# Optimization experiments

Hardware: AMD Instinct MI355X
Metric: run time of the kernel (lower is better)

## Reference

```python
import jax, jax.numpy as jnp
import numpy as np

N, E, CIN, COUT = 100000, 1600000, 64, 128
EPS = 1e-5  # torch BatchNorm default


def setup_inputs() -> dict:
    key = jax.random.key(0)
    ks = jax.random.split(key, 16)
    s = 0.1
    x = jax.random.normal(ks[0], (N, CIN), jnp.float32)
    src = jax.random.randint(ks[1], (E,), 0, N, dtype=jnp.int32)
    dst = jax.random.randint(ks[2], (E,), 0, N, dtype=jnp.int32)
    edge_index = jnp.stack([src, dst])  # [2, E]
    return {
        "x": x,
        "edge_index": edge_index,
        # conv0: GraphConv(CIN -> COUT)
        "W_root0": jax.random.normal(ks[3], (COUT, CIN), jnp.float32) * s,
        "W_nbr0": jax.random.normal(ks[4], (COUT, CIN), jnp.float32) * s,
        "b0": jnp.zeros((COUT,), jnp.float32),
        # bn0
        "g0": jnp.ones((COUT,), jnp.float32),
        "be0": jnp.zeros((COUT,), jnp.float32),
        # conv1: GraphConv(COUT -> COUT)
        "W_root1": jax.random.normal(ks[5], (COUT, COUT), jnp.float32) * s,
        "W_nbr1": jax.random.normal(ks[6], (COUT, COUT), jnp.float32) * s,
        "b1": jnp.zeros((COUT,), jnp.float32),
        # bn1
        "g1": jnp.ones((COUT,), jnp.float32),
        "be1": jnp.zeros((COUT,), jnp.float32),
        # residual 1x1 conv (Conv1d(CIN, COUT, 1))
        "Wlin": jax.random.normal(ks[7], (COUT, CIN), jnp.float32) * s,
        "blin": jnp.zeros((COUT,), jnp.float32),
    }


def graph_conv(x, src, dst, W_root, W_nbr, b):
    # PyG GraphConv: out_i = W_root x_i + W_nbr * sum_{j: (j->i) in E} x_j + b
    agg = jax.ops.segment_sum(x[src], dst, num_segments=N)  # scatter-add over edges
    return x @ W_root.T + agg @ W_nbr.T + b


def batch_norm(x, gamma, beta):
    # training-mode BatchNorm over the node dimension (biased variance)
    mu = jnp.mean(x, axis=0)
    var = jnp.mean(jnp.square(x - mu), axis=0)
    return (x - mu) * jax.lax.rsqrt(var + EPS) * gamma + beta


def reference(x, edge_index, W_root0, W_nbr0, b0, g0, be0,
              W_root1, W_nbr1, b1, g1, be1, Wlin, blin):
    src, dst = edge_index[0], edge_index[1]
    y = batch_norm(graph_conv(x, src, dst, W_root0, W_nbr0, b0), g0, be0)
    y = jax.nn.relu(y)
    y = batch_norm(graph_conv(y, src, dst, W_root1, W_nbr1, b1), g1, be1)
    out = y + (x @ Wlin.T + blin)  # 1x1 Conv1d residual projection
    return jax.nn.relu(out)
```

## Files before the change

### kernel.cpp

```cpp
#include <hip/hip_runtime.h>
#include <stdint.h>


#define CIN 64
#define COUT 128
#define BN_EPS 1e-5f
#define CURPAD 32
#define PCPAD 32
#define SPAD 32
#define PSH 8
#define PNODES (1 << PSH)
#define MAXP 512

typedef unsigned short u16;
typedef short short8 __attribute__((ext_vector_type(8)));
typedef float f32x4 __attribute__((ext_vector_type(4)));

__device__ __forceinline__ float bf2f(u16 u) {
    union { unsigned int i; float f; } v; v.i = ((unsigned int)u) << 16; return v.f;
}
__device__ __forceinline__ u16 f2bf(float f) {
    union { float f; unsigned int i; } v; v.f = f;
    unsigned int r = v.i + 0x7fffu + ((v.i >> 16) & 1u);
    return (u16)(r >> 16);
}
__device__ __forceinline__ float lo16(unsigned int w) { return bf2f((u16)(w & 0xffffu)); }
__device__ __forceinline__ float hi16(unsigned int w) { return bf2f((u16)(w >> 16)); }

template<bool BF> __device__ __forceinline__ float ldf(const void* p, long i) {
    if (BF) return bf2f(((const u16*)p)[i]);
    return ((const float*)p)[i];
}
template<bool BF> __device__ __forceinline__ short8 ld8(const void* p, long i) {
    if (BF) return *(const short8*)((const u16*)p + i);
    const float* f = (const float*)p + i;
    short8 r;
#pragma unroll
    for (int j = 0; j < 8; ++j) r[j] = (short)f2bf(f[j]);
    return r;
}

__device__ __forceinline__ void acc8(float* a, uint4 w) {
    a[0] += lo16(w.x); a[1] += hi16(w.x);
    a[2] += lo16(w.y); a[3] += hi16(w.y);
    a[4] += lo16(w.z); a[5] += hi16(w.z);
    a[6] += lo16(w.w); a[7] += hi16(w.w);
}

__global__ __launch_bounds__(256) void k_prep(const unsigned int* __restrict__ x,
        int* __restrict__ flag, const int* __restrict__ dst,
        int* __restrict__ pcount, int E, int np) {
    if (blockIdx.x == 0) {
        if (threadIdx.x < 64) {
            int lane = threadIdx.x;
            int cnt = 0;
#pragma unroll
            for (int i = 0; i < 8; ++i) {
                unsigned int w = x[lane * 8 + i];
                unsigned int e0 = (w >> 7) & 0xFFu, e1 = (w >> 23) & 0xFFu;
                cnt += (e0 >= 0x60u && e0 <= 0x8Eu);
                cnt += (e1 >= 0x60u && e1 <= 0x8Eu);
            }
            for (int o = 32; o; o >>= 1) cnt += __shfl_down(cnt, o);
            if (lane == 0) *flag = (cnt > 850) ? 1 : 0;
        }
        return;
    }
    __shared__ int h[MAXP];
    int bid = blockIdx.x - 1;
    int nb = gridDim.x - 1;
    for (int i = threadIdx.x; i < np; i += 256) h[i] = 0;
    __syncthreads();
    int stride = nb * 256;
    for (int e = bid * 256 + threadIdx.x; e < E; e += stride)
        atomicAdd(&h[dst[e] >> PSH], 1);
    __syncthreads();
    for (int i = threadIdx.x; i < np; i += 256)
        if (h[i]) atomicAdd(&pcount[i * PCPAD], h[i]);
}

__global__ void k_pscan(const int* __restrict__ pcount, int* __restrict__ pstart,
                        int* __restrict__ pcursor, int np, int E) {
    __shared__ int s[MAXP];
    int t = threadIdx.x;
    int v = (t < np) ? pcount[t * PCPAD] : 0;
    s[t] = v; __syncthreads();
    for (int o = 1; o < MAXP; o <<= 1) {
        int u = (t >= o) ? s[t - o] : 0;
        __syncthreads(); s[t] += u; __syncthreads();
    }
    if (t < np) {
        int ex = s[t] - v;
        pstart[t] = ex;
        pcursor[t * CURPAD] = ex;
    }
    if (t == 0) pstart[np] = E;
}

__global__ __launch_bounds__(256) void k_fill2(const int* __restrict__ src,
        const int* __restrict__ dst, int* __restrict__ pcursor,
        unsigned int* __restrict__ barr, int E, int np, int ntl,
        const int* __restrict__ flag, const void* __restrict__ x,
        u16* __restrict__ xb, long n8) {
    __shared__ int cnt[MAXP], gb[MAXP], loc[MAXP];
    int tid = threadIdx.x;
    if (blockIdx.x >= ntl) {
        int nb = gridDim.x - ntl;
        long idx = (long)(blockIdx.x - ntl) * 256 + tid;
        long stride = (long)nb * 256;
        uint4* d4 = (uint4*)xb;
        if (*flag) {
            const uint4* s4 = (const uint4*)x;
            for (; idx < n8; idx += stride) d4[idx] = s4[idx];
        } else {
            const float4* s4 = (const float4*)x;
            for (; idx < n8; idx += stride) {
                float4 a = s4[idx * 2], b = s4[idx * 2 + 1];
                uint4 o;
                o.x = (unsigned int)f2bf(a.x) | ((unsigned int)f2bf(a.y) << 16);
                o.y = (unsigned int)f2bf(a.z) | ((unsigned int)f2bf(a.w) << 16);
                o.z = (unsigned int)f2bf(b.x) | ((unsigned int)f2bf(b.y) << 16);
                o.w = (unsigned int)f2bf(b.z) | ((unsigned int)f2bf(b.w) << 16);
                d4[idx] = o;
            }
        }
        return;
    }
    int base = blockIdx.x * 4096;
    for (int i = tid; i < np; i += 256) { cnt[i] = 0; loc[i] = 0; }
    __syncthreads();
    int pk[16]; unsigned int rec[16];
#pragma unroll
    for (int k = 0; k < 16; ++k) {
        int e = base + k * 256 + tid;
        if (e < E) {
            int d = dst[e];
            pk[k] = d >> PSH;
            rec[k] = ((unsigned int)(d & (PNODES - 1)) << 20) | (unsigned int)src[e];
            atomicAdd(&cnt[pk[k]], 1);
        } else pk[k] = -1;
    }
    __syncthreads();
    for (int i = tid; i < np; i += 256)
        if (cnt[i]) gb[i] = atomicAdd(&pcursor[i * CURPAD], cnt[i]);
    __syncthreads();
#pragma unroll
    for (int k = 0; k < 16; ++k) {
        if (pk[k] >= 0) {
            int off = atomicAdd(&loc[pk[k]], 1);
            barr[gb[pk[k]] + off] = rec[k];
        }
    }
}

__global__ __launch_bounds__(256) void k_psort(const unsigned int* __restrict__ barr,
        const int* __restrict__ pstart, int* __restrict__ csr,
        int* __restrict__ row_start, int n, int np, int E) {
    __shared__ int hist[PNODES], curs[PNODES], tsum[256];
    int tid = threadIdx.x;
    int p = blockIdx.x;
    int e0 = pstart[p], e1 = pstart[p + 1];
    int node0 = p << PSH;
    hist[tid] = 0;
    __syncthreads();
    for (int t = e0 + tid; t < e1; t += 256)
        atomicAdd(&hist[barr[t] >> 20], 1);
    __syncthreads();
    int v = hist[tid];
    tsum[tid] = v; __syncthreads();
    for (int o = 1; o < 256; o <<= 1) {
        int u = (tid >= o) ? tsum[tid - o] : 0;
        __syncthreads(); tsum[tid] += u; __syncthreads();
    }
    int ex = tsum[tid] - v;
    curs[tid] = ex;
    int nd = node0 + tid;
    if (nd < n) row_start[nd] = e0 + ex;
    if (p == np - 1 && tid == 0) row_start[n] = E;
    __syncthreads();
    for (int t = e0 + tid; t < e1; t += 256) {
        unsigned int rec = barr[t];
        int pos = atomicAdd(&curs[rec >> 20], 1);
        csr[e0 + pos] = (int)(rec & 0xFFFFF);
    }
}

__global__ __launch_bounds__(256) void k_agg0(const u16* __restrict__ xb,
        const int* __restrict__ rs, const int* __restrict__ csr,
        u16* __restrict__ agg, int n) {
    int i = blockIdx.x * 4 + (threadIdx.x >> 6);
    if (i >= n) return;
    int lane = threadIdx.x & 63;
    int slot = lane >> 4, cp = lane & 15;
    const unsigned int* x32 = (const unsigned int*)xb;
    int b = rs[i], e = rs[i + 1];
    float acc[4] = {0.f, 0.f, 0.f, 0.f};
    int t = b + slot;
    for (; t + 12 < e; t += 16) {
        int j0 = csr[t], j1 = csr[t + 4], j2 = csr[t + 8], j3 = csr[t + 12];
        uint2 w0 = *((const uint2*)(x32 + (long)j0 * 32) + cp);
        uint2 w1 = *((const uint2*)(x32 + (long)j1 * 32) + cp);
        uint2 w2 = *((const uint2*)(x32 + (long)j2 * 32) + cp);
        uint2 w3 = *((const uint2*)(x32 + (long)j3 * 32) + cp);
        acc[0] += lo16(w0.x) + lo16(w1.x); acc[1] += hi16(w0.x) + hi16(w1.x);
        acc[2] += lo16(w0.y) + lo16(w1.y); acc[3] += hi16(w0.y) + hi16(w1.y);
        acc[0] += lo16(w2.x) + lo16(w3.x); acc[1] += hi16(w2.x) + hi16(w3.x);
        acc[2] += lo16(w2.y) + lo16(w3.y); acc[3] += hi16(w2.y) + hi16(w3.y);
    }
    for (; t < e; t += 4) {
        int j0 = csr[t];
        uint2 w0 = *((const uint2*)(x32 + (long)j0 * 32) + cp);
        acc[0] += lo16(w0.x); acc[1] += hi16(w0.x);
        acc[2] += lo16(w0.y); acc[3] += hi16(w0.y);
    }
#pragma unroll
    for (int k = 0; k < 4; ++k) {
        acc[k] += __shfl_xor(acc[k], 16);
        acc[k] += __shfl_xor(acc[k], 32);
    }
    if (slot == 0) {
        uint2 o;
        o.x = (unsigned int)f2bf(acc[0]) | ((unsigned int)f2bf(acc[1]) << 16);
        o.y = (unsigned int)f2bf(acc[2]) | ((unsigned int)f2bf(acc[3]) << 16);
        *((uint2*)((unsigned int*)agg + (long)i * 32) + cp) = o;
    }
}

__global__ __launch_bounds__(256) void k_y0p(unsigned int* __restrict__ y0,
        const float* __restrict__ sc, const float* __restrict__ sh, long nq) {
    long idx = (long)blockIdx.x * 256 + threadIdx.x;
    int colq = threadIdx.x & 15;
    float s8[8], h8[8];
#pragma unroll
    for (int j = 0; j < 8; ++j) { s8[j] = sc[colq * 8 + j]; h8[j] = sh[colq * 8 + j]; }
    long stride = (long)gridDim.x * 256;
    uint4* p = (uint4*)y0;
    for (; idx < nq; idx += stride) {
        uint4 w = p[idx];
        unsigned int r[4] = {w.x, w.y, w.z, w.w};
        uint4 o;
        unsigned int* po = (unsigned int*)&o;
#pragma unroll
        for (int d = 0; d < 4; ++d) {
            float a = fmaxf(lo16(r[d]) * s8[2 * d]     + h8[2 * d],     0.f);
            float b = fmaxf(hi16(r[d]) * s8[2 * d + 1] + h8[2 * d + 1], 0.f);
            po[d] = (unsigned int)f2bf(a) | ((unsigned int)f2bf(b) << 16);
        }
        p[idx] = o;
    }
}

__global__ __launch_bounds__(256) void k_agg1(const u16* __restrict__ y0p,
        const int* __restrict__ rs, const int* __restrict__ csr,
        u16* __restrict__ agg, int n) {
    int i = blockIdx.x * 4 + (threadIdx.x >> 6);
    if (i >= n) return;
    int lane = threadIdx.x & 63;
    int slot = lane >> 4, cp = lane & 15;
    const unsigned int* y32 = (const unsigned int*)y0p;
    int b = rs[i], e = rs[i + 1];
    float acc[8] = {0.f, 0.f, 0.f, 0.f, 0.f, 0.f, 0.f, 0.f};
    int t = b + slot;
    for (; t + 12 < e; t += 16) {
        int j0 = csr[t], j1 = csr[t + 4], j2 = csr[t + 8], j3 = csr[t + 12];
        uint4 w0 = *((const uint4*)(y32 + (long)j0 * 64) + cp);
        uint4 w1 = *((const uint4*)(y32 + (long)j1 * 64) + cp);
        uint4 w2 = *((const uint4*)(y32 + (long)j2 * 64) + cp);
        uint4 w3 = *((const uint4*)(y32 + (long)j3 * 64) + cp);
        acc8(acc, w0); acc8(acc, w1); acc8(acc, w2); acc8(acc, w3);
    }
    for (; t < e; t += 4) {
        int j0 = csr[t];
        uint4 w0 = *((const uint4*)(y32 + (long)j0 * 64) + cp);
        acc8(acc, w0);
    }
#pragma unroll
    for (int k = 0; k < 8; ++k) {
        acc[k] += __shfl_xor(acc[k], 16);
        acc[k] += __shfl_xor(acc[k], 32);
    }
    if (slot == 0) {
        uint4 o;
        o.x = (unsigned int)f2bf(acc[0]) | ((unsigned int)f2bf(acc[1]) << 16);
        o.y = (unsigned int)f2bf(acc[2]) | ((unsigned int)f2bf(acc[3]) << 16);
        o.z = (unsigned int)f2bf(acc[4]) | ((unsigned int)f2bf(acc[5]) << 16);
        o.w = (unsigned int)f2bf(acc[6]) | ((unsigned int)f2bf(acc[7]) << 16);
        *((uint4*)((unsigned int*)agg + (long)i * 64) + cp) = o;
    }
}

template<bool BF>
__device__ __forceinline__ void gemm0_impl(const u16* xb, const u16* agg,
                                           const void* Wr, const void* Wn,
                                           u16* y0, float* sumP, float* sqP,
                                           int n, int nch) {
    int tid = threadIdx.x;
    int wave = tid >> 6, lane = tid & 63, lr = lane & 15, q = lane >> 4;

    short8 wf[2][4];
#pragma unroll
    for (int i = 0; i < 2; ++i) {
        int c = (2 * wave + i) * 16 + lr;
#pragma unroll
        for (int ks = 0; ks < 4; ++ks) {
            const void* W = (ks < 2) ? Wr : Wn;
            wf[i][ks] = ld8<BF>(W, (long)c * CIN + (ks & 1) * 32 + q * 8);
        }
    }

    float st[2] = {0.f, 0.f}, sq[2] = {0.f, 0.f};
    for (int ch = blockIdx.x; ch < nch; ch += gridDim.x) {
        long chunk0 = (long)ch * 64;
#pragma unroll
        for (int t = 0; t < 4; ++t) {
            long rg = chunk0 + t * 16 + lr; if (rg > n - 1) rg = n - 1;
            short8 a[4];
#pragma unroll
            for (int ks = 0; ks < 2; ++ks)
                a[ks] = *(const short8*)(xb + rg * CIN + ks * 32 + q * 8);
#pragma unroll
            for (int ks = 0; ks < 2; ++ks)
                a[2 + ks] = *(const short8*)(agg + rg * CIN + ks * 32 + q * 8);
#pragma unroll
            for (int i = 0; i < 2; ++i) {
                f32x4 acc = {0.f, 0.f, 0.f, 0.f};
#pragma unroll
                for (int ks = 0; ks < 4; ++ks)
                    acc = __builtin_amdgcn_mfma_f32_16x16x32_bf16(a[ks], wf[i][ks], acc, 0, 0, 0);
                int c = (2 * wave + i) * 16 + lr;
#pragma unroll
                for (int r = 0; r < 4; ++r) {
                    long row = chunk0 + t * 16 + q * 4 + r;
                    if (row < n) {
                        y0[row * COUT + c] = f2bf(acc[r]);
                        st[i] += acc[r]; sq[i] += acc[r] * acc[r];
                    }
                }
            }
        }
    }
#pragma unroll
    for (int i = 0; i < 2; ++i) {
        st[i] += __shfl_xor(st[i], 16); st[i] += __shfl_xor(st[i], 32);
        sq[i] += __shfl_xor(sq[i], 16); sq[i] += __shfl_xor(sq[i], 32);
    }
    if (q == 0) {
#pragma unroll
        for (int i = 0; i < 2; ++i) {
            int c = (2 * wave + i) * 16 + lr;
            atomicAdd(&sumP[c * SPAD], st[i]);
            atomicAdd(&sqP[c * SPAD], sq[i]);
        }
    }
}

__global__ __launch_bounds__(256) void k_gemm0(const int* __restrict__ flag,
        const u16* __restrict__ xb, const u16* __restrict__ agg,
        const void* Wr, const void* Wn,
        u16* __restrict__ y0, float* __restrict__ sumP, float* __restrict__ sqP,
        int n, int nch) {
    if (*flag) gemm0_impl<true >(xb, agg, Wr, Wn, y0, sumP, sqP, n, nch);
    else       gemm0_impl<false>(xb, agg, Wr, Wn, y0, sumP, sqP, n, nch);
}

template<bool BF>
__device__ __forceinline__ void gemm1_impl(const u16* y0p, const u16* agg,
                                           const void* Wr, const void* Wn,
                                           u16* y1, float* sumP, float* sqP,
                                           int n, int nch) {
    int tid = threadIdx.x;
    int wave = tid >> 6, lane = tid & 63, lr = lane & 15, q = lane >> 4;

    short8 wf[2][8];
#pragma unroll
    for (int i = 0; i < 2; ++i) {
        int c = (2 * wave + i) * 16 + lr;
#pragma unroll
        for (int ks = 0; ks < 8; ++ks) {
            const void* W = (ks < 4) ? Wr : Wn;
            wf[i][ks] = ld8<BF>(W, (long)c * COUT + (ks & 3) * 32 + q * 8);
        }
    }

    float st[2] = {0.f, 0.f}, sq[2] = {0.f, 0.f};
    for (int ch = blockIdx.x; ch < nch; ch += gridDim.x) {
        long chunk0 = (long)ch * 64;
#pragma unroll
        for (int t = 0; t < 4; ++t) {
            long rg = chunk0 + t * 16 + lr; if (rg > n - 1) rg = n - 1;
            short8 a[8];
#pragma unroll
            for (int ks = 0; ks < 4; ++ks)
                a[ks] = *(const short8*)(y0p + rg * COUT + ks * 32 + q * 8);
#pragma unroll
            for (int ks = 0; ks < 4; ++ks)
                a[4 + ks] = *(const short8*)(agg + rg * COUT + ks * 32 + q * 8);
#pragma unroll
            for (int i = 0; i < 2; ++i) {
                f32x4 acc = {0.f, 0.f, 0.f, 0.f};
#pragma unroll
                for (int ks = 0; ks < 8; ++ks)
                    acc = __builtin_amdgcn_mfma_f32_16x16x32_bf16(a[ks], wf[i][ks], acc, 0, 0, 0);
                int c = (2 * wave + i) * 16 + lr;
#pragma unroll
                for (int r = 0; r < 4; ++r) {
                    long row = chunk0 + t * 16 + q * 4 + r;
                    if (row < n) {
                        y1[row * COUT + c] = f2bf(acc[r]);
                        st[i] += acc[r]; sq[i] += acc[r] * acc[r];
                    }
                }
            }
        }
    }
#pragma unroll
    for (int i = 0; i < 2; ++i) {
        st[i] += __shfl_xor(st[i], 16); st[i] += __shfl_xor(st[i], 32);
        sq[i] += __shfl_xor(sq[i], 16); sq[i] += __shfl_xor(sq[i], 32);
    }
    if (q == 0) {
#pragma unroll
        for (int i = 0; i < 2; ++i) {
            int c = (2 * wave + i) * 16 + lr;
            atomicAdd(&sumP[c * SPAD], st[i]);
            atomicAdd(&sqP[c * SPAD], sq[i]);
        }
    }
}

__global__ __launch_bounds__(256) void k_gemm1(const int* __restrict__ flag,
        const u16* __restrict__ y0p, const u16* __restrict__ agg,
        const void* Wr, const void* Wn,
        u16* y1_bf , u16* y1_ws,
        float* __restrict__ sumP, float* __restrict__ sqP, int n, int nch) {
    u16* y1 = *flag ? y1_bf : y1_ws;
    if (*flag) gemm1_impl<true >(y0p, agg, Wr, Wn, y1, sumP, sqP, n, nch);
    else       gemm1_impl<false>(y0p, agg, Wr, Wn, y1, sumP, sqP, n, nch);
}

__global__ void k_bnfin(const int* __restrict__ flag,
                        const float* __restrict__ sumP, const float* __restrict__ sqP,
                        const void* g, const void* be,
                        float* __restrict__ scale, float* __restrict__ shift, int n) {
    int c = threadIdx.x;
    bool bf = (*flag != 0);
    float inv = 1.f / (float)n;
    float mu = sumP[c * SPAD] * inv;
    float var = fmaxf(sqP[c * SPAD] * inv - mu * mu, 0.f);
    float gv = bf ? bf2f(((const u16*)g)[c]) : ((const float*)g)[c];
    float bv = bf ? bf2f(((const u16*)be)[c]) : ((const float*)be)[c];
    float sc = gv * rsqrtf(var + BN_EPS);
    scale[c] = sc;
    shift[c] = bv - mu * sc;
}

template<bool BF>
__device__ __forceinline__ void final_impl(const u16* xb, const u16* y1,
                                           const void* Wlin, const void* blin,
                                           const float* sc, const float* sh,
                                           void* out, int n, int nch, u16* lds) {
    const int ST = 130;
    int tid = threadIdx.x;
    int wave = tid >> 6, lane = tid & 63, lr = lane & 15, q = lane >> 4;

    short8 wf[2][2];
    float blc[2], scc[2], shc[2];
#pragma unroll
    for (int i = 0; i < 2; ++i) {
        int c = (2 * wave + i) * 16 + lr;
#pragma unroll
        for (int ks = 0; ks < 2; ++ks)
            wf[i][ks] = ld8<BF>(Wlin, (long)c * CIN + ks * 32 + q * 8);
        blc[i] = ldf<BF>(blin, c);
        scc[i] = sc[c]; shc[i] = sh[c];
    }

    const int rowy = tid >> 4, wy = tid & 15;
    short8 ry[4];

    auto regload = [&](long chunk0) {
#pragma unroll
        for (int i = 0; i < 4; ++i) {
            long rg = chunk0 + rowy + i * 16; if (rg > n - 1) rg = n - 1;
            ry[i] = *(const short8*)(y1 + rg * COUT + wy * 8);
        }
    };

    int ch = blockIdx.x;
    if (ch < nch) regload((long)ch * 64);
    for (; ch < nch; ch += gridDim.x) {
        long chunk0 = (long)ch * 64;
        __syncthreads();
#pragma unroll
        for (int i = 0; i < 4; ++i)
            *(short8*)(lds + (rowy + i * 16) * ST + wy * 8) = ry[i];
        __syncthreads();
        long nxt = (long)ch + gridDim.x;
        if (nxt < nch) regload(nxt * 64);

#pragma unroll
        for (int t = 0; t < 4; ++t) {
            long rg = chunk0 + t * 16 + lr; if (rg > n - 1) rg = n - 1;
            short8 a[2];
#pragma unroll
            for (int ks = 0; ks < 2; ++ks)
                a[ks] = *(const short8*)(xb + rg * CIN + ks * 32 + q * 8);
#pragma unroll
            for (int i = 0; i < 2; ++i) {
                f32x4 acc = {0.f, 0.f, 0.f, 0.f};
                acc = __builtin_amdgcn_mfma_f32_16x16x32_bf16(a[0], wf[i][0], acc, 0, 0, 0);
                acc = __builtin_amdgcn_mfma_f32_16x16x32_bf16(a[1], wf[i][1], acc, 0, 0, 0);
                int c = (2 * wave + i) * 16 + lr;
#pragma unroll
                for (int r = 0; r < 4; ++r) {
                    long row = chunk0 + t * 16 + q * 4 + r;
                    if (row < n) {
                        float yv = bf2f(lds[(t * 16 + q * 4 + r) * ST + c]);
                        float v = acc[r] + blc[i] + yv * scc[i] + shc[i];
                        v = fmaxf(v, 0.f);
                        if (BF) ((u16*)out)[row * COUT + c] = f2bf(v);
                        else    ((float*)out)[row * COUT + c] = v;
                    }
                }
            }
        }
    }
}

__global__ __launch_bounds__(256) void k_final(const int* __restrict__ flag,
        const u16* __restrict__ xb, const void* Wlin, const void* blin,
        const u16* y1_bf , const u16* y1_ws,
        const float* __restrict__ sc, const float* __restrict__ sh,
        void* out, int n, int nch) {
    __shared__ u16 lds[64 * 130];
    const u16* y1 = *flag ? y1_bf : y1_ws;
    if (*flag) final_impl<true >(xb, y1, Wlin, blin, sc, sh, out, n, nch, lds);
    else       final_impl<false>(xb, y1, Wlin, blin, sc, sh, out, n, nch, lds);
}

extern "C" void kernel_launch(void* const* d_in, const int* in_sizes, int n_in,
                              void* d_out, int out_size, void* d_ws, size_t ws_size,
                              hipStream_t stream) {
    (void)n_in; (void)out_size; (void)ws_size;
    const void* x    = d_in[0];
    const int*  ei   = (const int*)d_in[1];
    const void* Wr0  = d_in[2];
    const void* Wn0  = d_in[3];
    const void* g0   = d_in[5];
    const void* be0  = d_in[6];
    const void* Wr1  = d_in[7];
    const void* Wn1  = d_in[8];
    const void* g1   = d_in[10];
    const void* be1  = d_in[11];
    const void* Wlin = d_in[12];
    const void* blin = d_in[13];

    const int N = in_sizes[0] / CIN;
    const int E = in_sizes[1] / 2;
    const int* src = ei;
    const int* dst = ei + E;
    const int NP = (N + PNODES - 1) >> PSH;

    char* base = (char*)d_ws;
    size_t off = 0;
    auto carve = [&](size_t bytes) -> void* {
        void* p = base + off;
        off = (off + bytes + 255) & ~(size_t)255;
        return p;
    };
    int*   flag      = (int*)carve(256);
    int*   pcount    = (int*)carve(MAXP * PCPAD * sizeof(int));
    int*   pstart    = (int*)carve((MAXP + 1) * sizeof(int));
    int*   pcursor   = (int*)carve(MAXP * CURPAD * sizeof(int));
    float* statsP    = (float*)carve(4 * 128 * SPAD * sizeof(float));
    float* scsh      = (float*)carve(512 * sizeof(float));
    int*   row_start = (int*)carve((size_t)(N + 1) * sizeof(int));
    unsigned int* barr = (unsigned int*)carve((size_t)E * sizeof(int));
    int*   csr       = (int*)carve((size_t)E * sizeof(int));
    u16*   xb        = (u16*)carve((size_t)N * CIN * sizeof(u16));
    u16*   aggu      = (u16*)carve((size_t)N * COUT * sizeof(u16));
    u16*   y0        = (u16*)carve((size_t)N * COUT * sizeof(u16));
    u16*   y1_ws     = (u16*)carve((size_t)N * COUT * sizeof(u16));

    float* sum0P = statsP;
    float* sq0P  = statsP + 128 * SPAD;
    float* sum1P = statsP + 256 * SPAD;
    float* sq1P  = statsP + 384 * SPAD;

    hipMemsetAsync(pcount, 0, MAXP * PCPAD * sizeof(int), stream);
    hipMemsetAsync(statsP, 0, 4 * 128 * SPAD * sizeof(float), stream);

    const int nwb = (N + 3) / 4;
    const int nch = (N + 63) / 64;
    const int ntl = (E + 4095) / 4096;
    const int G   = nch < 1024 ? nch : 1024;
    const long nq = (long)N * 16;
    const long n8 = (long)N * CIN / 8;
    int g2 = (int)((nq + 255) / 256); if (g2 > 2048) g2 = 2048;
    int g3 = (int)((n8 + 255) / 256); if (g3 > 1024) g3 = 1024;

    k_prep<<<257, 256, 0, stream>>>((const unsigned int*)x, flag, dst, pcount, E, NP);
    k_pscan<<<1, MAXP, 0, stream>>>(pcount, pstart, pcursor, NP, E);
    k_fill2<<<ntl + g3, 256, 0, stream>>>(src, dst, pcursor, barr, E, NP, ntl,
                                          flag, x, xb, n8);
    k_psort<<<NP, 256, 0, stream>>>(barr, pstart, csr, row_start, N, NP, E);

    k_agg0 <<<nwb, 256, 0, stream>>>(xb, row_start, csr, aggu, N);
    k_gemm0<<<G, 256, 0, stream>>>(flag, xb, aggu, Wr0, Wn0, y0,
                                   sum0P, sq0P, N, nch);
    k_bnfin<<<1, 128, 0, stream>>>(flag, sum0P, sq0P, g0, be0,
                                   scsh, scsh + 128, N);

    k_y0p<<<g2, 256, 0, stream>>>((unsigned int*)y0, scsh, scsh + 128, nq);

    k_agg1 <<<nwb, 256, 0, stream>>>(y0, row_start, csr, aggu, N);
    k_gemm1<<<G, 256, 0, stream>>>(flag, y0, aggu, Wr1, Wn1,
                                   (u16*)d_out, y1_ws, sum1P, sq1P, N, nch);
    k_bnfin<<<1, 128, 0, stream>>>(flag, sum1P, sq1P, g1, be1,
                                   scsh + 256, scsh + 384, N);

    k_final<<<G, 256, 0, stream>>>(flag, xb, Wlin, blin,
                                   (const u16*)d_out, y1_ws,
                                   scsh + 256, scsh + 384, d_out, N, nch);
}
```

Before: 385.1 us.

## Fuse layer-1 neighbor aggregation into GEMM kernel via LDS staging

Removes the standalone k_agg1 kernel. The conv1 GEMM kernel now gathers and sums neighbor features for each 64-node chunk itself, stages the bf16 aggregate in shared memory (padded stride 130), and feeds the MFMA from LDS. This avoids writing the aggregate to global memory and reading it back, and saves one launch. The cost is that the gather now runs on the persistent GEMM grid G, with fewer waves in flight for latency hiding, and the gather and MFMA phases are serialized by barriers.

Result: slower. 414.4 us (+7.6%).

```diff
diff --git a/kernel.cpp b/kernel.cpp
--- a/kernel.cpp
+++ b/kernel.cpp
@@ -250,45 +250,6 @@
     }
 }
 
-__global__ __launch_bounds__(256) void k_agg1(const u16* __restrict__ y0p,
-        const int* __restrict__ rs, const int* __restrict__ csr,
-        u16* __restrict__ agg, int n) {
-    int i = blockIdx.x * 4 + (threadIdx.x >> 6);
-    if (i >= n) return;
-    int lane = threadIdx.x & 63;
-    int slot = lane >> 4, cp = lane & 15;
-    const unsigned int* y32 = (const unsigned int*)y0p;
-    int b = rs[i], e = rs[i + 1];
-    float acc[8] = {0.f, 0.f, 0.f, 0.f, 0.f, 0.f, 0.f, 0.f};
-    int t = b + slot;
-    for (; t + 12 < e; t += 16) {
-        int j0 = csr[t], j1 = csr[t + 4], j2 = csr[t + 8], j3 = csr[t + 12];
-        uint4 w0 = *((const uint4*)(y32 + (long)j0 * 64) + cp);
-        uint4 w1 = *((const uint4*)(y32 + (long)j1 * 64) + cp);
-        uint4 w2 = *((const uint4*)(y32 + (long)j2 * 64) + cp);
-        uint4 w3 = *((const uint4*)(y32 + (long)j3 * 64) + cp);
-        acc8(acc, w0); acc8(acc, w1); acc8(acc, w2); acc8(acc, w3);
-    }
-    for (; t < e; t += 4) {
-        int j0 = csr[t];
-        uint4 w0 = *((const uint4*)(y32 + (long)j0 * 64) + cp);
-        acc8(acc, w0);
-    }
-#pragma unroll
-    for (int k = 0; k < 8; ++k) {
-        acc[k] += __shfl_xor(acc[k], 16);
-        acc[k] += __shfl_xor(acc[k], 32);
-    }
-    if (slot == 0) {
-        uint4 o;
-        o.x = (unsigned int)f2bf(acc[0]) | ((unsigned int)f2bf(acc[1]) << 16);
-        o.y = (unsigned int)f2bf(acc[2]) | ((unsigned int)f2bf(acc[3]) << 16);
-        o.z = (unsigned int)f2bf(acc[4]) | ((unsigned int)f2bf(acc[5]) << 16);
-        o.w = (unsigned int)f2bf(acc[6]) | ((unsigned int)f2bf(acc[7]) << 16);
-        *((uint4*)((unsigned int*)agg + (long)i * 64) + cp) = o;
-    }
-}
-
 template<bool BF>
 __device__ __forceinline__ void gemm0_impl(const u16* xb, const u16* agg,
                                            const void* Wr, const void* Wn,
@@ -364,12 +325,17 @@
 }
 
 template<bool BF>
-__device__ __forceinline__ void gemm1_impl(const u16* y0p, const u16* agg,
-                                           const void* Wr, const void* Wn,
-                                           u16* y1, float* sumP, float* sqP,
-                                           int n, int nch) {
+__device__ __forceinline__ void ag1_impl(const u16* y0p,
+                                         const int* __restrict__ rs,
+                                         const int* __restrict__ csr,
+                                         const void* Wr, const void* Wn,
+                                         u16* y1, float* sumP, float* sqP,
+                                         int n, int nch, u16* lds) {
+    const int ST = 130;
     int tid = threadIdx.x;
     int wave = tid >> 6, lane = tid & 63, lr = lane & 15, q = lane >> 4;
+    int slot = lane >> 4, cp = lane & 15;
+    const unsigned int* y32 = (const unsigned int*)y0p;
 
     short8 wf[2][8];
 #pragma unroll
@@ -385,6 +351,40 @@
     float st[2] = {0.f, 0.f}, sq[2] = {0.f, 0.f};
     for (int ch = blockIdx.x; ch < nch; ch += gridDim.x) {
         long chunk0 = (long)ch * 64;
+        __syncthreads();
+        for (int j = 0; j < 16; ++j) {
+            int li = wave * 16 + j;
+            long node = chunk0 + li;
+            float acc[8] = {0.f, 0.f, 0.f, 0.f, 0.f, 0.f, 0.f, 0.f};
+            if (node < n) {
+                int b = rs[node], e = rs[node + 1];
+                int t = b + slot;
+                for (; t + 12 < e; t += 16) {
+                    int j0 = csr[t], j1 = csr[t + 4], j2 = csr[t + 8], j3 = csr[t + 12];
+                    uint4 w0 = *((const uint4*)(y32 + (long)j0 * 64) + cp);
+                    uint4 w1 = *((const uint4*)(y32 + (long)j1 * 64) + cp);
+                    uint4 w2 = *((const uint4*)(y32 + (long)j2 * 64) + cp);
+                    uint4 w3 = *((const uint4*)(y32 + (long)j3 * 64) + cp);
+                    acc8(acc, w0); acc8(acc, w1); acc8(acc, w2); acc8(acc, w3);
+                }
+                for (; t < e; t += 4) {
+                    uint4 w0 = *((const uint4*)(y32 + (long)csr[t] * 64) + cp);
+                    acc8(acc, w0);
+                }
+            }
+#pragma unroll
+            for (int k = 0; k < 8; ++k) {
+                acc[k] += __shfl_xor(acc[k], 16);
+                acc[k] += __shfl_xor(acc[k], 32);
+            }
+            if (slot == 0) {
+                short8 o;
+#pragma unroll
+                for (int k = 0; k < 8; ++k) o[k] = (short)f2bf(acc[k]);
+                *(short8*)(lds + li * ST + cp * 8) = o;
+            }
+        }
+        __syncthreads();
 #pragma unroll
         for (int t = 0; t < 4; ++t) {
             long rg = chunk0 + t * 16 + lr; if (rg > n - 1) rg = n - 1;
@@ -394,7 +394,7 @@
                 a[ks] = *(const short8*)(y0p + rg * COUT + ks * 32 + q * 8);
 #pragma unroll
             for (int ks = 0; ks < 4; ++ks)
-                a[4 + ks] = *(const short8*)(agg + rg * COUT + ks * 32 + q * 8);
+                a[4 + ks] = *(const short8*)(lds + (t * 16 + lr) * ST + ks * 32 + q * 8);
 #pragma unroll
             for (int i = 0; i < 2; ++i) {
                 f32x4 acc = {0.f, 0.f, 0.f, 0.f};
@@ -428,14 +428,15 @@
     }
 }
 
-__global__ __launch_bounds__(256) void k_gemm1(const int* __restrict__ flag,
-        const u16* __restrict__ y0p, const u16* __restrict__ agg,
-        const void* Wr, const void* Wn,
+__global__ __launch_bounds__(256) void k_ag1(const int* __restrict__ flag,
+        const u16* __restrict__ y0p, const int* __restrict__ rs,
+        const int* __restrict__ csr, const void* Wr, const void* Wn,
         u16* y1_bf , u16* y1_ws,
         float* __restrict__ sumP, float* __restrict__ sqP, int n, int nch) {
+    __shared__ u16 lds[64 * 130];
     u16* y1 = *flag ? y1_bf : y1_ws;
-    if (*flag) gemm1_impl<true >(y0p, agg, Wr, Wn, y1, sumP, sqP, n, nch);
-    else       gemm1_impl<false>(y0p, agg, Wr, Wn, y1, sumP, sqP, n, nch);
+    if (*flag) ag1_impl<true >(y0p, rs, csr, Wr, Wn, y1, sumP, sqP, n, nch, lds);
+    else       ag1_impl<false>(y0p, rs, csr, Wr, Wn, y1, sumP, sqP, n, nch, lds);
 }
 
 __global__ void k_bnfin(const int* __restrict__ flag,
@@ -613,9 +614,8 @@
 
     k_y0p<<<g2, 256, 0, stream>>>((unsigned int*)y0, scsh, scsh + 128, nq);
 
-    k_agg1 <<<nwb, 256, 0, stream>>>(y0, row_start, csr, aggu, N);
-    k_gemm1<<<G, 256, 0, stream>>>(flag, y0, aggu, Wr1, Wn1,
-                                   (u16*)d_out, y1_ws, sum1P, sq1P, N, nch);
+    k_ag1<<<G, 256, 0, stream>>>(flag, y0, row_start, csr, Wr1, Wn1,
+                                 (u16*)d_out, y1_ws, sum1P, sq1P, N, nch);
     k_bnfin<<<1, 128, 0, stream>>>(flag, sum1P, sq1P, g1, be1,
                                    scsh + 256, scsh + 384, N);
 
```

## Stage gemm1 input tiles through LDS with register prefetch of next chunk

Applied to the files above, without the earlier changes.

Before this change, every wave in the second GraphConv GEMM loaded the same 64-row y0/agg tile from global memory, so each block read its tile four times. Now the block loads each chunk once, cooperatively, into a padded LDS buffer, and the MFMA operands are read from LDS. The next chunk is prefetched into registers while the current one is computed. This costs an extra LDS buffer of about 33 KB plus two barriers per chunk, which lowers occupancy. The 258-element row stride also leaves the 16-byte LDS accesses not 16-byte aligned, which may split or slow those accesses.

Measured after the change: 376.8 us. -2.2%, faster.

```diff
diff --git a/kernel.cpp b/kernel.cpp
--- a/kernel.cpp
+++ b/kernel.cpp
@@ -367,7 +367,8 @@
 __device__ __forceinline__ void gemm1_impl(const u16* y0p, const u16* agg,
                                            const void* Wr, const void* Wn,
                                            u16* y1, float* sumP, float* sqP,
-                                           int n, int nch) {
+                                           int n, int nch, u16* lds) {
+    const int ST = 258;
     int tid = threadIdx.x;
     int wave = tid >> 6, lane = tid & 63, lr = lane & 15, q = lane >> 4;
 
@@ -382,19 +383,38 @@
         }
     }
 
+    const int rowy = tid >> 4, wy = tid & 15;
+    short8 ry[4], rag[4];
+    auto regload = [&](long chunk0) {
+#pragma unroll
+        for (int i = 0; i < 4; ++i) {
+            long rg = chunk0 + rowy + i * 16; if (rg > n - 1) rg = n - 1;
+            ry[i]  = *(const short8*)(y0p + rg * COUT + wy * 8);
+            rag[i] = *(const short8*)(agg + rg * COUT + wy * 8);
+        }
+    };
+
     float st[2] = {0.f, 0.f}, sq[2] = {0.f, 0.f};
-    for (int ch = blockIdx.x; ch < nch; ch += gridDim.x) {
+    int ch = blockIdx.x;
+    if (ch < nch) regload((long)ch * 64);
+    for (; ch < nch; ch += gridDim.x) {
         long chunk0 = (long)ch * 64;
+        __syncthreads();
+#pragma unroll
+        for (int i = 0; i < 4; ++i) {
+            *(short8*)(lds + (rowy + i * 16) * ST + wy * 8) = ry[i];
+            *(short8*)(lds + (rowy + i * 16) * ST + 128 + wy * 8) = rag[i];
+        }
+        __syncthreads();
+        long nxt = (long)ch + gridDim.x;
+        if (nxt < nch) regload(nxt * 64);
+
 #pragma unroll
         for (int t = 0; t < 4; ++t) {
-            long rg = chunk0 + t * 16 + lr; if (rg > n - 1) rg = n - 1;
             short8 a[8];
 #pragma unroll
-            for (int ks = 0; ks < 4; ++ks)
-                a[ks] = *(const short8*)(y0p + rg * COUT + ks * 32 + q * 8);
-#pragma unroll
-            for (int ks = 0; ks < 4; ++ks)
-                a[4 + ks] = *(const short8*)(agg + rg * COUT + ks * 32 + q * 8);
+            for (int ks = 0; ks < 8; ++ks)
+                a[ks] = *(const short8*)(lds + (t * 16 + lr) * ST + ks * 32 + q * 8);
 #pragma unroll
             for (int i = 0; i < 2; ++i) {
                 f32x4 acc = {0.f, 0.f, 0.f, 0.f};
@@ -433,9 +453,10 @@
         const void* Wr, const void* Wn,
         u16* y1_bf , u16* y1_ws,
         float* __restrict__ sumP, float* __restrict__ sqP, int n, int nch) {
+    __shared__ u16 lds[64 * 258];
     u16* y1 = *flag ? y1_bf : y1_ws;
-    if (*flag) gemm1_impl<true >(y0p, agg, Wr, Wn, y1, sumP, sqP, n, nch);
-    else       gemm1_impl<false>(y0p, agg, Wr, Wn, y1, sumP, sqP, n, nch);
+    if (*flag) gemm1_impl<true >(y0p, agg, Wr, Wn, y1, sumP, sqP, n, nch, lds);
+    else       gemm1_impl<false>(y0p, agg, Wr, Wn, y1, sumP, sqP, n, nch, lds);
 }
 
 __global__ void k_bnfin(const int* __restrict__ flag,
```
